# Kernel optimization log

Measured on AMD Instinct MI355X. Metric: run time of the kernel, lower is better.

## Reference

```python
import jax, jax.numpy as jnp
import numpy as np

EPS = 1e-5

def setup_inputs() -> dict:
    key = jax.random.key(0)
    ks = jax.random.split(key, 6)
    B, S, F, D = 512, 64, 768, 256
    # xavier-ish scales for weights
    return {
        "audio_feat": jax.random.normal(ks[0], (B, S, F), dtype=jnp.float32),
        "visual_feat": jax.random.normal(ks[1], (B, S, F), dtype=jnp.float32),
        "Wa": jax.random.normal(ks[2], (F, D), dtype=jnp.float32) * (1.0 / np.sqrt(F)),
        "ba": jnp.zeros((D,), dtype=jnp.float32),
        "Wv": jax.random.normal(ks[3], (F, D), dtype=jnp.float32) * (1.0 / np.sqrt(F)),
        "bv": jnp.zeros((D,), dtype=jnp.float32),
        "corr": jax.random.normal(ks[4], (D, D), dtype=jnp.float32) * float(np.sqrt(2.0 / (D + D))),
        "Wb": jax.random.normal(ks[5], (2 * D, 64), dtype=jnp.float32) * (1.0 / np.sqrt(2 * D)),
        "bb": jnp.zeros((64,), dtype=jnp.float32),
        "gamma": jnp.ones((64,), dtype=jnp.float32),
        "beta": jnp.zeros((64,), dtype=jnp.float32),
    }


def reference(audio_feat, visual_feat, Wa, ba, Wv, bv, corr, Wb, bb, gamma, beta):
    # project: [b,s,768] -> [b,s,256]
    a = jnp.einsum('bsf,fd->bsd', audio_feat, Wa) + ba      # audio proj
    v = jnp.einsum('bsf,fd->bsd', visual_feat, Wv) + bv     # vision proj
    vT = jnp.swapaxes(v, 1, 2)                              # [b,d,s]
    # bilinear correlation: cc[b,i,j] = a[b,i,:] @ corr @ v[b,j,:]
    cc = jnp.einsum('bid,de,bje->bij', a, corr, v)          # [b,sa,sv]
    audio_att = jax.nn.softmax(cc, axis=1)                  # softmax over audio positions
    visual_att = jax.nn.softmax(cc, axis=2)                 # softmax over visual positions (of cc^T along dim 1)
    # attended features, both [b,d,s]
    att_a = jnp.einsum('bid,bij->bdj', a, audio_att) + jnp.swapaxes(a, 1, 2)
    att_v = jnp.einsum('bdj,bij->bdi', vT, jnp.swapaxes(visual_att, 1, 2))
    # note: bmm(vT [b,d,sv], visual_att^T' ...) -> torch does vT @ visual_att_t where
    # visual_att_t[b,j,i] = visual_att[b,i,j]; equivalent einsum below
    att_v = jnp.einsum('bdj,bji->bdi', vT, jnp.swapaxes(visual_att, 1, 2)) + vT
    fused = jnp.concatenate([att_a, att_v], axis=1)         # [b,2d,s]
    fused = jnp.swapaxes(fused, 1, 2)                       # [b,s,2d]
    h = jnp.einsum('bsk,ko->bso', fused, Wb) + bb           # [b,s,64]
    mu = jnp.mean(h, axis=-1, keepdims=True)
    var = jnp.mean(jnp.square(h - mu), axis=-1, keepdims=True)
    h = (h - mu) * jax.lax.rsqrt(var + EPS) * gamma + beta
    return jax.nn.relu(h)
```

## Files before the change

kernel.cpp:

```cpp
#include <hip/hip_runtime.h>

typedef _Float16 f16x8 __attribute__((ext_vector_type(8)));
typedef _Float16 f16x4 __attribute__((ext_vector_type(4)));
typedef float    f32x4 __attribute__((ext_vector_type(4)));

#define A16_OFF   0u
#define V16_OFF   16777216u
#define WAP_OFF   33554432u
#define WVP_OFF   33947648u
#define CORRT_OFF 34340864u
#define WBT_OFF   34471936u

#define SCHED0() __builtin_amdgcn_sched_barrier(0)
#define SBAR()   __builtin_amdgcn_s_barrier()

__device__ __forceinline__ void gl_lds16(const void* g, void* l) {
    __builtin_amdgcn_global_load_lds(
        (const __attribute__((address_space(1))) void*)g,
        (__attribute__((address_space(3))) void*)l, 16, 0, 0);
}

__global__ __launch_bounds__(256) void k_prep(
    const float* __restrict__ Wa, const float* __restrict__ Wv,
    const float* __restrict__ corr, const float* __restrict__ Wb,
    _Float16* __restrict__ WaP, _Float16* __restrict__ WvP,
    _Float16* __restrict__ corrT, _Float16* __restrict__ WbT)
{
    __shared__ _Float16 tile[64][72];
    int bid = blockIdx.x;
    int t = threadIdx.x;
    if (bid < 192) {
        int z = bid >= 96;
        int b = z ? bid - 96 : bid;
        const float* W = z ? Wv : Wa;
        _Float16* P = z ? WvP : WaP;
        int kc = b >> 2, nbg = b & 3;
        int l = t & 63, sub = t >> 6;
        int nb = nbg * 4 + sub;
        int q = l >> 4, lm = l & 15;
        int k0 = kc * 32 + q * 8;
        int n = nb * 16 + lm;
        _Float16 tmp[8];
        #pragma unroll
        for (int e = 0; e < 8; ++e)
            tmp[e] = (_Float16)W[(size_t)(k0 + e) * 256 + n];
        *reinterpret_cast<f16x8*>(P + ((size_t)(kc * 16 + nb) * 64 + l) * 8) =
            *reinterpret_cast<const f16x8*>(tmp);
    } else {
        int b2 = bid - 192;
        const float* src; _Float16* dst; int R, C, tr, tc;
        if (b2 < 16) { src = corr; dst = corrT; R = 256; C = 256; tr = b2 >> 2; tc = b2 & 3; }
        else         { src = Wb;   dst = WbT;   R = 512; C = 64;  tr = b2 - 16; tc = 0;      }
        int r0 = tr * 64, c0 = tc * 64;
        #pragma unroll
        for (int it = 0; it < 16; ++it) {
            int idx = t + it * 256;
            int r = idx >> 6, c = idx & 63;
            tile[r][c] = (_Float16)src[(size_t)(r0 + r) * C + (c0 + c)];
        }
        __syncthreads();
        #pragma unroll
        for (int it = 0; it < 16; ++it) {
            int idx = t + it * 256;
            int c = idx >> 6, r = idx & 63;
            dst[(size_t)(c0 + c) * R + (r0 + r)] = tile[r][c];
        }
    }
}

__global__ __launch_bounds__(512, 4) void k_proj(
    const float* __restrict__ Xa, const float* __restrict__ Xv,
    const _Float16* __restrict__ WaP, const _Float16* __restrict__ WvP,
    const float* __restrict__ ba, const float* __restrict__ bv,
    _Float16* __restrict__ Aout, _Float16* __restrict__ Vout)
{
    __shared__ __align__(16) char smem[65536];

    const int bid = blockIdx.x;
    const int z = bid >> 8, mb = bid & 255;
    const float*    X    = z ? Xv  : Xa;
    const _Float16* WP   = z ? WvP : WaP;
    const float*    bias = z ? bv  : ba;
    _Float16*       Out  = z ? Vout : Aout;
    const int m0 = mb * 128;

    const int t = threadIdx.x, lane = t & 63, w = t >> 6;
    const int wr = w >> 1, wc = w & 1;
    const int q = lane >> 4, lm = lane & 15;

    f32x4 acc[2][8] = {};

    auto stageA = [&](int ks, int buf) {
        char* base = smem + buf * 16384;
        #pragma unroll
        for (int it = 0; it < 2; ++it) {
            int idx = t + it * 512;
            int r = idx >> 3, c = idx & 7;
            int gc = c ^ (r & 7);
            char* l = base + (it * 512 + w * 64) * 16;
            gl_lds16(X + (size_t)(m0 + r) * 768 + ks * 32 + gc * 4, l);
        }
    };
    auto stageB = [&](int ks, int buf) {
        char* base = smem + 32768 + buf * 16384;
        #pragma unroll
        for (int it = 0; it < 2; ++it) {
            int idx = t + it * 512;
            char* l = base + (it * 512 + w * 64) * 16;
            gl_lds16(WP + ((size_t)ks * 1024 + idx) * 8, l);
        }
    };

    stageA(0, 0); stageB(0, 0);
    stageA(1, 1); stageB(1, 1);
    asm volatile("s_waitcnt vmcnt(4)" ::: "memory"); SCHED0();
    SBAR();

    for (int ks = 0; ks < 24; ++ks) {
        const int cur = ks & 1;
        const char* Ac = smem + cur * 16384;
        const char* Bc = smem + 32768 + cur * 16384;

        f16x8 af[2];
        #pragma unroll
        for (int mf = 0; mf < 2; ++mf) {
            int r = wr * 32 + mf * 16 + lm;
            const char* base = Ac + r * 128;
            int c0 = (2 * q) ^ (r & 7);
            int c1 = (2 * q + 1) ^ (r & 7);
            f32x4 lo = *reinterpret_cast<const f32x4*>(base + c0 * 16);
            f32x4 hi = *reinterpret_cast<const f32x4*>(base + c1 * 16);
            f16x4 l4 = __builtin_convertvector(lo, f16x4);
            f16x4 h4 = __builtin_convertvector(hi, f16x4);
            af[mf] = __builtin_shufflevector(l4, h4, 0, 1, 2, 3, 4, 5, 6, 7);
        }
        #pragma unroll
        for (int nf = 0; nf < 8; ++nf) {
            int nb = wc * 8 + nf;
            f16x8 bf = *reinterpret_cast<const f16x8*>(Bc + (nb * 64 + lane) * 16);
            acc[0][nf] = __builtin_amdgcn_mfma_f32_16x16x32_f16(af[0], bf, acc[0][nf], 0, 0, 0);
            acc[1][nf] = __builtin_amdgcn_mfma_f32_16x16x32_f16(af[1], bf, acc[1][nf], 0, 0, 0);
        }
        asm volatile("s_waitcnt lgkmcnt(0)" ::: "memory"); SCHED0();
        SBAR();
        if (ks + 2 < 24) { stageA(ks + 2, cur); stageB(ks + 2, cur); }
        if (ks < 22) { asm volatile("s_waitcnt vmcnt(4)" ::: "memory"); }
        else         { asm volatile("s_waitcnt vmcnt(0)" ::: "memory"); }
        SCHED0();
        SBAR();
    }

    float biasv[8];
    #pragma unroll
    for (int nf = 0; nf < 8; ++nf)
        biasv[nf] = bias[wc * 128 + nf * 16 + lm];

    _Float16* Cs = (_Float16*)smem;
    #pragma unroll
    for (int mf = 0; mf < 2; ++mf)
        #pragma unroll
        for (int nf = 0; nf < 8; ++nf)
            #pragma unroll
            for (int r = 0; r < 4; ++r)
                Cs[(wr * 32 + mf * 16 + q * 4 + r) * 256 + wc * 128 + nf * 16 + lm] =
                    (_Float16)(acc[mf][nf][r] + biasv[nf]);
    __syncthreads();
    #pragma unroll
    for (int it = 0; it < 8; ++it) {
        int idx = t + it * 512;
        int row = idx >> 5, c = idx & 31;
        f16x8 vv = *reinterpret_cast<const f16x8*>(Cs + row * 256 + c * 8);
        *reinterpret_cast<f16x8*>(Out + (size_t)(m0 + row) * 256 + c * 8) = vv;
    }
}

#define SM_A    0u
#define SM_V    33792u
#define SM_AC   67584u
#define SM_CC   101376u
#define SM_ATA  118272u
#define SM_ATV  127488u
#define SM_AWT  136704u
#define SM_VWT  145920u
#define SM_RED  155136u
#define SM_TOTAL 159232u

__global__ __launch_bounds__(256) void k_fuse(
    const _Float16* __restrict__ A16, const _Float16* __restrict__ V16,
    const _Float16* __restrict__ corrT, const _Float16* __restrict__ WbT,
    const float* __restrict__ bb, const float* __restrict__ gamma,
    const float* __restrict__ beta, float* __restrict__ out)
{
    extern __shared__ char sm[];
    _Float16* a_s   = (_Float16*)(sm + SM_A);
    _Float16* v_s   = (_Float16*)(sm + SM_V);
    _Float16* ac_s  = (_Float16*)(sm + SM_AC);
    float*    cc_s  = (float*)(sm + SM_CC);
    _Float16* attAT = (_Float16*)(sm + SM_ATA);
    _Float16* attV  = (_Float16*)(sm + SM_ATV);
    _Float16* awT   = (_Float16*)(sm + SM_AWT);
    _Float16* vwT   = (_Float16*)(sm + SM_VWT);
    float*    red   = (float*)(sm + SM_RED);

    const int b = blockIdx.x;
    const int t = threadIdx.x, lane = t & 63, w = t >> 6;
    const int q = lane >> 4, lm = lane & 15;

    const _Float16* Ab = A16 + (size_t)b * 64 * 256;
    const _Float16* Vb = V16 + (size_t)b * 64 * 256;
    #pragma unroll
    for (int it = 0; it < 8; ++it) {
        int idx = t + it * 256;
        int row = idx >> 5, kc = idx & 31;
        *reinterpret_cast<f16x8*>(a_s + row * 264 + kc * 8) =
            *reinterpret_cast<const f16x8*>(Ab + row * 256 + kc * 8);
        *reinterpret_cast<f16x8*>(v_s + row * 264 + kc * 8) =
            *reinterpret_cast<const f16x8*>(Vb + row * 256 + kc * 8);
    }
    __syncthreads();

    {
        f32x4 acc[4][4] = {};
        for (int ks = 0; ks < 8; ++ks) {
            f16x8 af[4];
            #pragma unroll
            for (int mf = 0; mf < 4; ++mf)
                af[mf] = *reinterpret_cast<const f16x8*>(a_s + (mf * 16 + lm) * 264 + ks * 32 + q * 8);
            #pragma unroll
            for (int nf = 0; nf < 4; ++nf) {
                int e = w * 64 + nf * 16 + lm;
                f16x8 bf = *reinterpret_cast<const f16x8*>(corrT + (size_t)e * 256 + ks * 32 + q * 8);
                #pragma unroll
                for (int mf = 0; mf < 4; ++mf)
                    acc[mf][nf] = __builtin_amdgcn_mfma_f32_16x16x32_f16(af[mf], bf, acc[mf][nf], 0, 0, 0);
            }
        }
        #pragma unroll
        for (int mf = 0; mf < 4; ++mf)
            #pragma unroll
            for (int nf = 0; nf < 4; ++nf)
                #pragma unroll
                for (int r = 0; r < 4; ++r)
                    ac_s[(mf * 16 + 4 * q + r) * 264 + (w * 64 + nf * 16 + lm)] = (_Float16)acc[mf][nf][r];
    }
    __syncthreads();

    {
        f32x4 acc[4] = {};
        for (int ks = 0; ks < 8; ++ks) {
            f16x8 bf = *reinterpret_cast<const f16x8*>(v_s + (w * 16 + lm) * 264 + ks * 32 + q * 8);
            #pragma unroll
            for (int mf = 0; mf < 4; ++mf) {
                f16x8 af = *reinterpret_cast<const f16x8*>(ac_s + (mf * 16 + lm) * 264 + ks * 32 + q * 8);
                acc[mf] = __builtin_amdgcn_mfma_f32_16x16x32_f16(af, bf, acc[mf], 0, 0, 0);
            }
        }
        #pragma unroll
        for (int mf = 0; mf < 4; ++mf)
            #pragma unroll
            for (int r = 0; r < 4; ++r)
                cc_s[(mf * 16 + 4 * q + r) * 66 + (w * 16 + lm)] = acc[mf][r];
    }
    __syncthreads();

    {
        int j = t & 63, seg = w;
        float cmx = -1e30f, rmx = -1e30f;
        #pragma unroll
        for (int k = 0; k < 16; ++k) {
            int i = seg * 16 + k;
            cmx = fmaxf(cmx, cc_s[i * 66 + j]);
            rmx = fmaxf(rmx, cc_s[j * 66 + i]);
        }
        red[0 * 256 + seg * 64 + j] = cmx;
        red[2 * 256 + seg * 64 + j] = rmx;
        __syncthreads();
        float cm = fmaxf(fmaxf(red[0 * 256 + 0 * 64 + j], red[0 * 256 + 1 * 64 + j]),
                         fmaxf(red[0 * 256 + 2 * 64 + j], red[0 * 256 + 3 * 64 + j]));
        float rm = fmaxf(fmaxf(red[2 * 256 + 0 * 64 + j], red[2 * 256 + 1 * 64 + j]),
                         fmaxf(red[2 * 256 + 2 * 64 + j], red[2 * 256 + 3 * 64 + j]));
        float cs = 0.f, rs = 0.f;
        #pragma unroll
        for (int k = 0; k < 16; ++k) {
            int i = seg * 16 + k;
            cs += __expf(cc_s[i * 66 + j] - cm);
            rs += __expf(cc_s[j * 66 + i] - rm);
        }
        red[1 * 256 + seg * 64 + j] = cs;
        red[3 * 256 + seg * 64 + j] = rs;
        __syncthreads();
        float csum = red[1 * 256 + 0 * 64 + j] + red[1 * 256 + 1 * 64 + j] +
                     red[1 * 256 + 2 * 64 + j] + red[1 * 256 + 3 * 64 + j];
        float rsum = red[3 * 256 + 0 * 64 + j] + red[3 * 256 + 1 * 64 + j] +
                     red[3 * 256 + 2 * 64 + j] + red[3 * 256 + 3 * 64 + j];
        float cinv = 1.f / csum, rinv = 1.f / rsum;
        #pragma unroll
        for (int k = 0; k < 16; ++k) {
            int i = seg * 16 + k;
            float pa = __expf(cc_s[i * 66 + j] - cm) * cinv;
            if (i == j) pa += 1.f;
            attAT[j * 72 + i] = (_Float16)pa;
            float pv = __expf(cc_s[j * 66 + i] - rm) * rinv;
            if (i == j) pv += 1.f;
            attV[j * 72 + i] = (_Float16)pv;
        }
    }

    {
        int isV = w >> 1, wcol = w & 1;
        const _Float16* src = isV ? v_s : a_s;
        const int doff = isV ? 256 : 0;
        f32x4 acc[4][2] = {};
        for (int ks = 0; ks < 8; ++ks) {
            f16x8 af[4];
            #pragma unroll
            for (int mf = 0; mf < 4; ++mf)
                af[mf] = *reinterpret_cast<const f16x8*>(src + (mf * 16 + lm) * 264 + ks * 32 + q * 8);
            #pragma unroll
            for (int nf = 0; nf < 2; ++nf) {
                int o = wcol * 32 + nf * 16 + lm;
                f16x8 bf = *reinterpret_cast<const f16x8*>(WbT + (size_t)o * 512 + doff + ks * 32 + q * 8);
                #pragma unroll
                for (int mf = 0; mf < 4; ++mf)
                    acc[mf][nf] = __builtin_amdgcn_mfma_f32_16x16x32_f16(af[mf], bf, acc[mf][nf], 0, 0, 0);
            }
        }
        _Float16* dst = isV ? vwT : awT;
        #pragma unroll
        for (int mf = 0; mf < 4; ++mf)
            #pragma unroll
            for (int nf = 0; nf < 2; ++nf)
                #pragma unroll
                for (int r = 0; r < 4; ++r)
                    dst[(wcol * 32 + nf * 16 + lm) * 72 + (mf * 16 + 4 * q + r)] = (_Float16)acc[mf][nf][r];
    }
    __syncthreads();

    f32x4 hacc[4] = {};
    #pragma unroll
    for (int kk = 0; kk < 2; ++kk) {
        f16x8 a1 = *reinterpret_cast<const f16x8*>(attAT + (16 * w + lm) * 72 + kk * 32 + q * 8);
        f16x8 a2 = *reinterpret_cast<const f16x8*>(attV  + (16 * w + lm) * 72 + kk * 32 + q * 8);
        #pragma unroll
        for (int nf = 0; nf < 4; ++nf) {
            f16x8 b1 = *reinterpret_cast<const f16x8*>(awT + (nf * 16 + lm) * 72 + kk * 32 + q * 8);
            f16x8 b2 = *reinterpret_cast<const f16x8*>(vwT + (nf * 16 + lm) * 72 + kk * 32 + q * 8);
            hacc[nf] = __builtin_amdgcn_mfma_f32_16x16x32_f16(a1, b1, hacc[nf], 0, 0, 0);
            hacc[nf] = __builtin_amdgcn_mfma_f32_16x16x32_f16(a2, b2, hacc[nf], 0, 0, 0);
        }
    }

    {
        float bbv[4], gv[4], bev[4];
        #pragma unroll
        for (int nf = 0; nf < 4; ++nf) {
            int o = nf * 16 + lm;
            bbv[nf] = bb[o]; gv[nf] = gamma[o]; bev[nf] = beta[o];
        }
        #pragma unroll
        for (int r = 0; r < 4; ++r) {
            float vals[4]; float s1 = 0.f, s2 = 0.f;
            #pragma unroll
            for (int nf = 0; nf < 4; ++nf) {
                float hv = hacc[nf][r] + bbv[nf];
                vals[nf] = hv; s1 += hv; s2 += hv * hv;
            }
            #pragma unroll
            for (int m = 1; m < 16; m <<= 1) {
                s1 += __shfl_xor(s1, m, 64);
                s2 += __shfl_xor(s2, m, 64);
            }
            float mu = s1 * 0.015625f;
            float var = s2 * 0.015625f - mu * mu;
            float rstd = rsqrtf(var + 1e-5f);
            int s = 16 * w + 4 * q + r;
            float* orow = out + ((size_t)b * 64 + s) * 64;
            #pragma unroll
            for (int nf = 0; nf < 4; ++nf) {
                float y = (vals[nf] - mu) * rstd * gv[nf] + bev[nf];
                orow[nf * 16 + lm] = fmaxf(y, 0.f);
            }
        }
    }
}

extern "C" void kernel_launch(void* const* d_in, const int* in_sizes, int n_in,
                              void* d_out, int out_size, void* d_ws, size_t ws_size,
                              hipStream_t stream) {
    const float* Xa    = (const float*)d_in[0];
    const float* Xv    = (const float*)d_in[1];
    const float* Wa    = (const float*)d_in[2];
    const float* ba    = (const float*)d_in[3];
    const float* Wv    = (const float*)d_in[4];
    const float* bv    = (const float*)d_in[5];
    const float* corr  = (const float*)d_in[6];
    const float* Wb    = (const float*)d_in[7];
    const float* bb    = (const float*)d_in[8];
    const float* gamma = (const float*)d_in[9];
    const float* beta  = (const float*)d_in[10];
    float* out = (float*)d_out;
    char* ws = (char*)d_ws;

    _Float16* a16   = (_Float16*)(ws + A16_OFF);
    _Float16* v16   = (_Float16*)(ws + V16_OFF);
    _Float16* WaP   = (_Float16*)(ws + WAP_OFF);
    _Float16* WvP   = (_Float16*)(ws + WVP_OFF);
    _Float16* corrT = (_Float16*)(ws + CORRT_OFF);
    _Float16* WbT   = (_Float16*)(ws + WBT_OFF);

    hipLaunchKernelGGL(k_prep, dim3(216), dim3(256), 0, stream,
                       Wa, Wv, corr, Wb, WaP, WvP, corrT, WbT);
    hipLaunchKernelGGL(k_proj, dim3(512), dim3(512), 0, stream,
                       Xa, Xv, WaP, WvP, ba, bv, a16, v16);
    (void)hipFuncSetAttribute((const void*)k_fuse,
                              hipFuncAttributeMaxDynamicSharedMemorySize, SM_TOTAL);
    hipLaunchKernelGGL(k_fuse, dim3(512), dim3(256), SM_TOTAL, stream,
                       a16, v16, corrT, WbT, bb, gamma, beta, out);
}
```

Measured before the change: 87.29 us.

## Restructure projection GEMM pipeline with larger K-steps and dynamic LDS

The projection kernel now stages K in chunks of 96 instead of 32, giving 8 outer iterations instead of 24 and fewer barriers and waits. The A tile stays double-buffered (96 KB) and the B tile uses a single 48 KB buffer in dynamic shared memory, 144 KB in total. Block indices are remapped so that consecutive blocks are interleaved across groups of eight. The larger LDS footprint limits occupancy to one block per CU. The single B buffer is reloaded between barriers, which serializes part of the weight fetch.

```diff
diff --git a/kernel.cpp b/kernel.cpp
--- a/kernel.cpp
+++ b/kernel.cpp
@@ -68,16 +68,19 @@
     }
 }
 
-__global__ __launch_bounds__(512, 4) void k_proj(
+__global__ __launch_bounds__(512, 2) void k_proj(
     const float* __restrict__ Xa, const float* __restrict__ Xv,
     const _Float16* __restrict__ WaP, const _Float16* __restrict__ WvP,
     const float* __restrict__ ba, const float* __restrict__ bv,
     _Float16* __restrict__ Aout, _Float16* __restrict__ Vout)
 {
-    __shared__ __align__(16) char smem[65536];
+    extern __shared__ __align__(16) char sm7[];
+    char* Asm = sm7;
+    char* Bsm = sm7 + 98304;
 
     const int bid = blockIdx.x;
-    const int z = bid >> 8, mb = bid & 255;
+    const int lin = (bid & 7) * 64 + (bid >> 3);
+    const int z = lin >> 8, mb = lin & 255;
     const float*    X    = z ? Xv  : Xa;
     const _Float16* WP   = z ? WvP : WaP;
     const float*    bias = z ? bv  : ba;
@@ -91,63 +94,65 @@
     f32x4 acc[2][8] = {};
 
     auto stageA = [&](int ks, int buf) {
-        char* base = smem + buf * 16384;
-        #pragma unroll
-        for (int it = 0; it < 2; ++it) {
-            int idx = t + it * 512;
-            int r = idx >> 3, c = idx & 7;
-            int gc = c ^ (r & 7);
-            char* l = base + (it * 512 + w * 64) * 16;
-            gl_lds16(X + (size_t)(m0 + r) * 768 + ks * 32 + gc * 4, l);
+        char* base = Asm + buf * 49152;
+        #pragma unroll
+        for (int it = 0; it < 6; ++it) {
+            int idx0 = w * 384 + it * 64;
+            int idx = idx0 + lane;
+            int row = idx / 24, cw = idx % 24;
+            int gc = (cw & 24) | ((cw & 7) ^ (row & 7));
+            gl_lds16(X + (size_t)(m0 + row) * 768 + ks * 96 + gc * 4,
+                     base + idx0 * 16);
         }
     };
-    auto stageB = [&](int ks, int buf) {
-        char* base = smem + 32768 + buf * 16384;
-        #pragma unroll
-        for (int it = 0; it < 2; ++it) {
-            int idx = t + it * 512;
-            char* l = base + (it * 512 + w * 64) * 16;
-            gl_lds16(WP + ((size_t)ks * 1024 + idx) * 8, l);
+    auto stageB = [&](int ks) {
+        #pragma unroll
+        for (int it = 0; it < 6; ++it) {
+            int idx0 = w * 384 + it * 64;
+            gl_lds16(WP + ((size_t)ks * 3072 + idx0 + lane) * 8,
+                     Bsm + idx0 * 16);
         }
     };
 
-    stageA(0, 0); stageB(0, 0);
-    stageA(1, 1); stageB(1, 1);
-    asm volatile("s_waitcnt vmcnt(4)" ::: "memory"); SCHED0();
+    stageA(0, 0); stageB(0); stageA(1, 1);
+    asm volatile("s_waitcnt vmcnt(6)" ::: "memory"); SCHED0();
     SBAR();
 
-    for (int ks = 0; ks < 24; ++ks) {
-        const int cur = ks & 1;
-        const char* Ac = smem + cur * 16384;
-        const char* Bc = smem + 32768 + cur * 16384;
-
-        f16x8 af[2];
-        #pragma unroll
-        for (int mf = 0; mf < 2; ++mf) {
-            int r = wr * 32 + mf * 16 + lm;
-            const char* base = Ac + r * 128;
-            int c0 = (2 * q) ^ (r & 7);
-            int c1 = (2 * q + 1) ^ (r & 7);
-            f32x4 lo = *reinterpret_cast<const f32x4*>(base + c0 * 16);
-            f32x4 hi = *reinterpret_cast<const f32x4*>(base + c1 * 16);
-            f16x4 l4 = __builtin_convertvector(lo, f16x4);
-            f16x4 h4 = __builtin_convertvector(hi, f16x4);
-            af[mf] = __builtin_shufflevector(l4, h4, 0, 1, 2, 3, 4, 5, 6, 7);
-        }
-        #pragma unroll
-        for (int nf = 0; nf < 8; ++nf) {
-            int nb = wc * 8 + nf;
-            f16x8 bf = *reinterpret_cast<const f16x8*>(Bc + (nb * 64 + lane) * 16);
-            acc[0][nf] = __builtin_amdgcn_mfma_f32_16x16x32_f16(af[0], bf, acc[0][nf], 0, 0, 0);
-            acc[1][nf] = __builtin_amdgcn_mfma_f32_16x16x32_f16(af[1], bf, acc[1][nf], 0, 0, 0);
+    #pragma unroll
+    for (int ks = 0; ks < 8; ++ks) {
+        const char* Ac = Asm + (ks & 1) * 49152;
+        #pragma unroll
+        for (int kk = 0; kk < 3; ++kk) {
+            f16x8 af[2];
+            #pragma unroll
+            for (int mf = 0; mf < 2; ++mf) {
+                int r = wr * 32 + mf * 16 + lm;
+                int c0 = kk * 8 + q * 2;
+                int s0 = (kk * 8) | ((q * 2) ^ (r & 7));
+                int s1 = (kk * 8) | ((q * 2 + 1) ^ (r & 7));
+                (void)c0;
+                f32x4 lo = *reinterpret_cast<const f32x4*>(Ac + r * 384 + s0 * 16);
+                f32x4 hi = *reinterpret_cast<const f32x4*>(Ac + r * 384 + s1 * 16);
+                f16x4 l4 = __builtin_convertvector(lo, f16x4);
+                f16x4 h4 = __builtin_convertvector(hi, f16x4);
+                af[mf] = __builtin_shufflevector(l4, h4, 0, 1, 2, 3, 4, 5, 6, 7);
+            }
+            #pragma unroll
+            for (int nf = 0; nf < 8; ++nf) {
+                f16x8 bf = *reinterpret_cast<const f16x8*>(
+                    Bsm + (kk * 1024 + (wc * 8 + nf) * 64 + lane) * 16);
+                acc[0][nf] = __builtin_amdgcn_mfma_f32_16x16x32_f16(af[0], bf, acc[0][nf], 0, 0, 0);
+                acc[1][nf] = __builtin_amdgcn_mfma_f32_16x16x32_f16(af[1], bf, acc[1][nf], 0, 0, 0);
+            }
         }
         asm volatile("s_waitcnt lgkmcnt(0)" ::: "memory"); SCHED0();
         SBAR();
-        if (ks + 2 < 24) { stageA(ks + 2, cur); stageB(ks + 2, cur); }
-        if (ks < 22) { asm volatile("s_waitcnt vmcnt(4)" ::: "memory"); }
-        else         { asm volatile("s_waitcnt vmcnt(0)" ::: "memory"); }
+        if (ks < 7) stageB(ks + 1);
+        if (ks < 6) stageA(ks + 2, ks & 1);
+        if (ks < 6)      { asm volatile("s_waitcnt vmcnt(6)" ::: "memory"); }
+        else if (ks == 6){ asm volatile("s_waitcnt vmcnt(0)" ::: "memory"); }
         SCHED0();
-        SBAR();
+        if (ks < 7) SBAR();
     }
 
     float biasv[8];
@@ -155,7 +160,8 @@
     for (int nf = 0; nf < 8; ++nf)
         biasv[nf] = bias[wc * 128 + nf * 16 + lm];
 
-    _Float16* Cs = (_Float16*)smem;
+    __syncthreads();
+    _Float16* Cs = (_Float16*)Asm;
     #pragma unroll
     for (int mf = 0; mf < 2; ++mf)
         #pragma unroll
@@ -410,7 +416,9 @@
 
     hipLaunchKernelGGL(k_prep, dim3(216), dim3(256), 0, stream,
                        Wa, Wv, corr, Wb, WaP, WvP, corrT, WbT);
-    hipLaunchKernelGGL(k_proj, dim3(512), dim3(512), 0, stream,
+    (void)hipFuncSetAttribute((const void*)k_proj,
+                              hipFuncAttributeMaxDynamicSharedMemorySize, 147456);
+    hipLaunchKernelGGL(k_proj, dim3(512), dim3(512), 147456, stream,
                        Xa, Xv, WaP, WvP, ba, bv, a16, v16);
     (void)hipFuncSetAttribute((const void*)k_fuse,
                               hipFuncAttributeMaxDynamicSharedMemorySize, SM_TOTAL);
```

New measurement: 101.7 us. 1.17x slower.
